# Kernel tuning notes

Hardware: AMD Instinct MI355X
Metric: run time of the kernel (lower is better)

Reference implementation:

```python
import jax, jax.numpy as jnp
import numpy as np

EMB_DIM = 1024
N_HEADS = 16
HEAD_DIM = EMB_DIM // N_HEADS
WINDOW = 128
B, T = 4, 2048


def setup_inputs() -> dict:
    key = jax.random.key(0)
    k1, k2, k3 = jax.random.split(key, 3)
    x = jax.random.normal(k1, (B, T, EMB_DIM), dtype=jnp.float32)
    # nn.Linear weights: stored as [out, in], applied as x @ W^T
    s1 = 1.0 / np.sqrt(EMB_DIM)
    w_qkv = jax.random.uniform(k2, (3 * EMB_DIM, EMB_DIM), jnp.float32, -s1, s1)
    w_out = jax.random.uniform(k3, (EMB_DIM, EMB_DIM), jnp.float32, -s1, s1)
    return {"x": x, "w_qkv": w_qkv, "w_out": w_out}


def reference(x, w_qkv, w_out):
    Bs, Ts, C = x.shape
    scale = HEAD_DIM ** -0.5
    qkv = x @ w_qkv.T                                   # [B,T,3C]
    qkv = qkv.reshape(Bs, Ts, 3, N_HEADS, HEAD_DIM)
    qkv = jnp.transpose(qkv, (2, 0, 3, 1, 4))           # [3,B,H,T,D]
    q, k, v = qkv[0], qkv[1], qkv[2]
    scores = jnp.einsum('bhtd,bhsd->bhts', q, k) * scale  # [B,H,T,T]
    i = jnp.arange(Ts)[:, None]
    j = jnp.arange(Ts)[None, :]
    # causal AND within sliding window: i - WINDOW <= j <= i
    allowed = (j <= i) & (j >= i - WINDOW)               # [T,T] bool
    scores = jnp.where(allowed[None, None], scores, -jnp.inf)
    attn = jax.nn.softmax(scores, axis=-1)
    out = jnp.einsum('bhts,bhsd->bhtd', attn, v)         # [B,H,T,D]
    out = jnp.transpose(out, (0, 2, 1, 3)).reshape(Bs, Ts, C)
    return out @ w_out.T
```

## Files before the change

kernel.cpp:

```cpp
#include <hip/hip_runtime.h>
#include <hip/hip_bf16.h>
#include <stdint.h>

typedef __attribute__((ext_vector_type(8))) short bf16x8;
typedef __attribute__((ext_vector_type(4))) float f32x4;
typedef __attribute__((ext_vector_type(4))) unsigned short u16x4;

#define B_ 4
#define T_ 2048
#define C_ 1024
#define H_ 16
#define D_ 64

__device__ __forceinline__ unsigned short f2bf(float f) {
  union { float f; uint32_t u; } v; v.f = f;
  uint32_t u = v.u;
  uint32_t r = (u + 0x7FFFu + ((u >> 16) & 1u)) >> 16;
  return (unsigned short)r;
}

__global__ void __launch_bounds__(256) cast_all(const float* __restrict__ x,
                                                const float* __restrict__ wqkv,
                                                const float* __restrict__ wout,
                                                unsigned short* __restrict__ xb,
                                                unsigned short* __restrict__ wqkvb,
                                                unsigned short* __restrict__ woutb) {
  int bid = blockIdx.x;
  const float* src; unsigned short* dst; int i;
  if (bid < 8192)       { src = x;    dst = xb;    i = bid * 256 + threadIdx.x; }
  else if (bid < 11264) { src = wqkv; dst = wqkvb; i = (bid - 8192) * 256 + threadIdx.x; }
  else                  { src = wout; dst = woutb; i = (bid - 11264) * 256 + threadIdx.x; }
  float4 f = ((const float4*)src)[i];
  u16x4 o;
  o[0] = f2bf(f.x); o[1] = f2bf(f.y); o[2] = f2bf(f.z); o[3] = f2bf(f.w);
  ((u16x4*)dst)[i] = o;
}

__global__ void __launch_bounds__(256, 2) gemm_qkv(const unsigned short* __restrict__ A,
                                                   const unsigned short* __restrict__ Bm,
                                                   unsigned short* __restrict__ qb,
                                                   unsigned short* __restrict__ kb,
                                                   unsigned short* __restrict__ vb) {
  __shared__ short lds[24576];
  const int tid = threadIdx.x;
  const int bm = blockIdx.y * 256;
  const int bn = blockIdx.x * 128;

  const int wave = tid >> 6;
  const int l = tid & 63;
  const int wm = wave >> 1, wn = wave & 1;
  const int lm = l & 15, lq = l >> 4;
  const int lr = l >> 2;
  const int lc = (l & 3) << 3;

  f32x4 acc[8][4];
#pragma unroll
  for (int i = 0; i < 8; i++)
#pragma unroll
    for (int j = 0; j < 4; j++) acc[i][j] = (f32x4){0.f, 0.f, 0.f, 0.f};

  const unsigned short* gs[6];
  int ldo[6];
#pragma unroll
  for (int i = 0; i < 6; i++) {
    int c = wave * 6 + i;
    if (c < 16) {
      gs[i] = A + (size_t)(bm + 16 * c + lr) * 1024 + lc;
      ldo[i] = c * 512;
    } else {
      gs[i] = Bm + (size_t)(bn + 16 * (c - 16) + lr) * 1024 + lc;
      ldo[i] = 8192 + (c - 16) * 512;
    }
  }

#define STAGE(curb, kk)                                                          \
  do {                                                                           \
    _Pragma("unroll")                                                            \
    for (int i = 0; i < 6; i++) {                                                \
      __builtin_amdgcn_global_load_lds(                                          \
          (__attribute__((address_space(1))) void*)(uintptr_t)(const void*)(gs[i] + (kk)), \
          (__attribute__((address_space(3))) void*)(lds + ldo[i] + (curb) * 12288),        \
          16, 0, 0);                                                             \
    }                                                                            \
  } while (0)

  STAGE(0, 0);
  int cur = 0;
  __syncthreads();

  for (int k0 = 0; k0 < 1024; k0 += 32) {
    if (k0 + 32 < 1024) STAGE(cur ^ 1, k0 + 32);
    const short* As_ = lds + cur * 12288;
    const short* Bs_ = lds + cur * 12288 + 8192;
    bf16x8 Bf[4];
#pragma unroll
    for (int j = 0; j < 4; j++)
      Bf[j] = *(const bf16x8*)&Bs_[(wn * 64 + 16 * j + lm) * 32 + 8 * lq];
#pragma unroll
    for (int h = 0; h < 2; h++) {
      bf16x8 Af[4];
#pragma unroll
      for (int i = 0; i < 4; i++)
        Af[i] = *(const bf16x8*)&As_[(wm * 128 + 64 * h + 16 * i + lm) * 32 + 8 * lq];
#pragma unroll
      for (int i = 0; i < 4; i++)
#pragma unroll
        for (int j = 0; j < 4; j++)
          acc[4 * h + i][j] =
              __builtin_amdgcn_mfma_f32_16x16x32_bf16(Af[i], Bf[j], acc[4 * h + i][j], 0, 0, 0);
    }
    __syncthreads();
    cur ^= 1;
  }
#undef STAGE

  if (bn >= 2048) {
#pragma unroll
    for (int h = 0; h < 2; h++)
#pragma unroll
      for (int i = 0; i < 4; i++)
#pragma unroll
        for (int j = 0; j < 4; j++) {
          int m0 = bm + wm * 128 + 64 * h + 16 * i + 4 * lq;
          int n = (bn - 2048) + wn * 64 + 16 * j + lm;
          int hh = n >> 6, d = n & 63;
          int b = m0 >> 11, t = m0 & 2047;
          u16x4 o;
#pragma unroll
          for (int r = 0; r < 4; r++) o[r] = f2bf(acc[4 * h + i][j][r]);
          *(u16x4*)&vb[(((size_t)(b * 16 + hh)) * 64 + d) * 2048 + t] = o;
        }
  } else {
#pragma unroll
    for (int p = 0; p < 2; ++p) {
      if (p) __syncthreads();
      if (wm == p) {
#pragma unroll
        for (int h = 0; h < 2; h++)
#pragma unroll
          for (int i = 0; i < 4; i++)
#pragma unroll
            for (int j = 0; j < 4; j++)
#pragma unroll
              for (int r = 0; r < 4; r++)
                lds[(64 * h + 16 * i + 4 * lq + r) * 132 + wn * 64 + 16 * j + lm] =
                    (short)f2bf(acc[4 * h + i][j][r]);
      }
      __syncthreads();
#pragma unroll
      for (int k = 0; k < 8; k++) {
        int c = tid + 256 * k;
        int row = c >> 4;
        int col = (c & 15) << 3;
        bf16x8 v = *(const bf16x8*)&lds[row * 132 + col];
        int m = bm + 128 * p + row, n = bn + col;
        int which = n >> 10, rem = n & 1023;
        int hh = rem >> 6, d = rem & 63;
        int b = m >> 11, t = m & 2047;
        unsigned short* dst = (which == 0) ? qb : kb;
        *(bf16x8*)&dst[(((size_t)(b * 16 + hh)) * 2048 + t) * 64 + d] = v;
      }
    }
  }
}

__global__ void __launch_bounds__(256) gemm_out(const unsigned short* __restrict__ A,
                                                const unsigned short* __restrict__ Bm,
                                                float* __restrict__ fo) {
  __shared__ short lds[16384];
  const int tid = threadIdx.x;
  const int bm = blockIdx.y * 128;
  const int bn = blockIdx.x * 128;
  const int wave = tid >> 6;
  const int l = tid & 63;
  const int wm = wave >> 1, wn = wave & 1;
  const int lm = l & 15, lq = l >> 4;
  const int lr = l >> 2;
  const int lc = (l & 3) << 3;

  f32x4 acc[4][4];
#pragma unroll
  for (int i = 0; i < 4; i++)
#pragma unroll
    for (int j = 0; j < 4; j++) acc[i][j] = (f32x4){0.f, 0.f, 0.f, 0.f};

  const unsigned short* gsrc[4];
  int ldoff[4];
#pragma unroll
  for (int i = 0; i < 4; i++) {
    int c = wave * 4 + i;
    if (c < 8) {
      gsrc[i] = A + (size_t)(bm + 16 * c + lr) * 1024 + lc;
      ldoff[i] = (16 * c) * 32;
    } else {
      gsrc[i] = Bm + (size_t)(bn + 16 * (c - 8) + lr) * 1024 + lc;
      ldoff[i] = 8192 + (16 * (c - 8)) * 32;
    }
  }

#define STAGE(curb, kk)                                                          \
  do {                                                                           \
    _Pragma("unroll")                                                            \
    for (int i = 0; i < 4; i++) {                                                \
      __builtin_amdgcn_global_load_lds(                                          \
          (__attribute__((address_space(1))) void*)(uintptr_t)(const void*)(gsrc[i] + (kk)), \
          (__attribute__((address_space(3))) void*)(lds + ldoff[i] + (curb) * 4096),         \
          16, 0, 0);                                                             \
    }                                                                            \
  } while (0)

  STAGE(0, 0);
  int cur = 0;
  __syncthreads();

  for (int k0 = 0; k0 < 1024; k0 += 32) {
    if (k0 + 32 < 1024) STAGE(cur ^ 1, k0 + 32);
    bf16x8 af[4], bfr[4];
#pragma unroll
    for (int i = 0; i < 4; i++)
      af[i] = *(const bf16x8*)&lds[cur * 4096 + (wm * 64 + 16 * i + lm) * 32 + 8 * lq];
#pragma unroll
    for (int j = 0; j < 4; j++)
      bfr[j] = *(const bf16x8*)&lds[8192 + cur * 4096 + (wn * 64 + 16 * j + lm) * 32 + 8 * lq];
#pragma unroll
    for (int i = 0; i < 4; i++)
#pragma unroll
      for (int j = 0; j < 4; j++)
        acc[i][j] = __builtin_amdgcn_mfma_f32_16x16x32_bf16(af[i], bfr[j], acc[i][j], 0, 0, 0);
    __syncthreads();
    cur ^= 1;
  }
#undef STAGE

#pragma unroll
  for (int i = 0; i < 4; i++)
#pragma unroll
    for (int j = 0; j < 4; j++)
#pragma unroll
      for (int r = 0; r < 4; r++) {
        int m = bm + wm * 64 + 16 * i + 4 * lq + r;
        int n = bn + wn * 64 + 16 * j + lm;
        fo[(size_t)m * 1024 + n] = acc[i][j][r];
      }
}

__global__ void __launch_bounds__(256) attn_swa(const unsigned short* __restrict__ Qb,
                                               const unsigned short* __restrict__ Kb,
                                               const unsigned short* __restrict__ Vt,
                                               unsigned short* __restrict__ Ob) {
  __shared__ short P[4][16 * 40];
  const int wv = threadIdx.x >> 6;
  const int l = threadIdx.x & 63;
  const int wid = blockIdx.x * 4 + wv;
  const int bh = wid >> 7;
  const int t0 = (wid & 127) << 4;
  const int lm = l & 15, lq = l >> 4;
  const size_t base = (size_t)bh * (T_ * D_);

  bf16x8 aq0 = *(const bf16x8*)(Qb + base + (size_t)(t0 + lm) * 64 + 8 * lq);
  bf16x8 aq1 = *(const bf16x8*)(Qb + base + (size_t)(t0 + lm) * 64 + 32 + 8 * lq);

  float mst[4], lst[4];
  f32x4 Oa[4];
#pragma unroll
  for (int r = 0; r < 4; r++) { mst[r] = -1e30f; lst[r] = 0.f; }
#pragma unroll
  for (int jt = 0; jt < 4; jt++) Oa[jt] = (f32x4){0.f, 0.f, 0.f, 0.f};

  const float cs = 0.125f * 1.44269504f;
  int jstart = t0 - 128; if (jstart < 0) jstart = 0;

  for (int j0 = jstart; j0 < t0 + 16; j0 += 32) {
    f32x4 S[2];
#pragma unroll
    for (int hh = 0; hh < 2; hh++) {
      int kr = j0 + 16 * hh + lm; if (kr > T_ - 1) kr = T_ - 1;
      bf16x8 bk0 = *(const bf16x8*)(Kb + base + (size_t)kr * 64 + 8 * lq);
      bf16x8 bk1 = *(const bf16x8*)(Kb + base + (size_t)kr * 64 + 32 + 8 * lq);
      f32x4 s = (f32x4){0.f, 0.f, 0.f, 0.f};
      s = __builtin_amdgcn_mfma_f32_16x16x32_bf16(aq0, bk0, s, 0, 0, 0);
      s = __builtin_amdgcn_mfma_f32_16x16x32_bf16(aq1, bk1, s, 0, 0, 0);
      S[hh] = s;
    }
    float p0s[4], p1s[4], al[4];
#pragma unroll
    for (int r = 0; r < 4; r++) {
      int t = t0 + 4 * lq + r;
      int ja = j0 + lm, jb = j0 + 16 + lm;
      float s0 = ((ja <= t) && (ja + 128 >= t)) ? S[0][r] * cs : -1e30f;
      float s1 = ((jb <= t) && (jb + 128 >= t)) ? S[1][r] * cs : -1e30f;
      float m2 = fmaxf(s0, s1);
#pragma unroll
      for (int off = 1; off < 16; off <<= 1) m2 = fmaxf(m2, __shfl_xor(m2, off));
      float mn = fmaxf(mst[r], m2);
      float a = __builtin_amdgcn_exp2f(mst[r] - mn);
      float p0 = __builtin_amdgcn_exp2f(s0 - mn);
      float p1 = __builtin_amdgcn_exp2f(s1 - mn);
      float ps = p0 + p1;
#pragma unroll
      for (int off = 1; off < 16; off <<= 1) ps += __shfl_xor(ps, off);
      lst[r] = lst[r] * a + ps;
      mst[r] = mn;
      al[r] = a; p0s[r] = p0; p1s[r] = p1;
    }
#pragma unroll
    for (int jt = 0; jt < 4; jt++)
#pragma unroll
      for (int r = 0; r < 4; r++) Oa[jt][r] *= al[r];
#pragma unroll
    for (int r = 0; r < 4; r++) {
      P[wv][(4 * lq + r) * 40 + lm] = (short)f2bf(p0s[r]);
      P[wv][(4 * lq + r) * 40 + 16 + lm] = (short)f2bf(p1s[r]);
    }
    bf16x8 pa = *(const bf16x8*)&P[wv][lm * 40 + 8 * lq];
#pragma unroll
    for (int jt = 0; jt < 4; jt++) {
      bf16x8 vf = *(const bf16x8*)(Vt + base + (size_t)(16 * jt + lm) * 2048 + j0 + 8 * lq);
      Oa[jt] = __builtin_amdgcn_mfma_f32_16x16x32_bf16(pa, vf, Oa[jt], 0, 0, 0);
    }
  }
  const int b = bh >> 4, h = bh & 15;
#pragma unroll
  for (int r = 0; r < 4; r++) {
    float inv = 1.0f / lst[r];
    int t = t0 + 4 * lq + r;
#pragma unroll
    for (int jt = 0; jt < 4; jt++) {
      int c = h * 64 + 16 * jt + lm;
      Ob[((size_t)(b * T_ + t)) * 1024 + c] = f2bf(Oa[jt][r] * inv);
    }
  }
}

extern "C" void kernel_launch(void* const* d_in, const int* in_sizes, int n_in,
                              void* d_out, int out_size, void* d_ws, size_t ws_size,
                              hipStream_t stream) {
  const float* x = (const float*)d_in[0];
  const float* w_qkv = (const float*)d_in[1];
  const float* w_out = (const float*)d_in[2];
  float* out = (float*)d_out;

  unsigned short* xb = (unsigned short*)d_ws;
  unsigned short* wqkvb = xb + (size_t)8192 * 1024;
  unsigned short* woutb = wqkvb + (size_t)3072 * 1024;
  unsigned short* qb = woutb + (size_t)1024 * 1024;
  unsigned short* kb = qb + (size_t)64 * 2048 * 64;
  unsigned short* vb = kb + (size_t)64 * 2048 * 64;

  cast_all<<<12288, 256, 0, stream>>>(x, w_qkv, w_out, xb, wqkvb, woutb);

  gemm_qkv<<<dim3(24, 32), 256, 0, stream>>>(xb, wqkvb, qb, kb, vb);

  attn_swa<<<2048, 256, 0, stream>>>(qb, kb, vb, xb);

  gemm_out<<<dim3(8, 64), 256, 0, stream>>>(xb, woutb, out);
}
```

Before: 229.9 us.

## Process four query tiles per wave in sliding-window attention to reuse K/V loads

Each attention wave now handles 64 query rows as four 16-row tiles instead of one, so every loaded K and V fragment feeds up to four MFMA tiles, with per-tile activity masks skipping fully masked tiles. This cuts redundant global K/V reads but raises register pressure and shrinks the grid to 512 blocks, which may lower occupancy. The QKV GEMM launch is also split into two half-height launches via a row-offset argument, which adds a launch without an obvious speed benefit.

```diff
diff --git a/kernel.cpp b/kernel.cpp
--- a/kernel.cpp
+++ b/kernel.cpp
@@ -40,10 +40,11 @@
                                                    const unsigned short* __restrict__ Bm,
                                                    unsigned short* __restrict__ qb,
                                                    unsigned short* __restrict__ kb,
-                                                   unsigned short* __restrict__ vb) {
+                                                   unsigned short* __restrict__ vb,
+                                                   int bm0) {
   __shared__ short lds[24576];
   const int tid = threadIdx.x;
-  const int bm = blockIdx.y * 256;
+  const int bm = bm0 + blockIdx.y * 256;
   const int bn = blockIdx.x * 128;
 
   const int wave = tid >> 6;
@@ -248,88 +249,119 @@
                                                const unsigned short* __restrict__ Kb,
                                                const unsigned short* __restrict__ Vt,
                                                unsigned short* __restrict__ Ob) {
-  __shared__ short P[4][16 * 40];
+  __shared__ short P[4][64 * 40];
   const int wv = threadIdx.x >> 6;
   const int l = threadIdx.x & 63;
   const int wid = blockIdx.x * 4 + wv;
-  const int bh = wid >> 7;
-  const int t0 = (wid & 127) << 4;
+  const int bh = wid >> 5;
+  const int t0 = (wid & 31) << 6;
   const int lm = l & 15, lq = l >> 4;
   const size_t base = (size_t)bh * (T_ * D_);
 
-  bf16x8 aq0 = *(const bf16x8*)(Qb + base + (size_t)(t0 + lm) * 64 + 8 * lq);
-  bf16x8 aq1 = *(const bf16x8*)(Qb + base + (size_t)(t0 + lm) * 64 + 32 + 8 * lq);
-
-  float mst[4], lst[4];
-  f32x4 Oa[4];
-#pragma unroll
-  for (int r = 0; r < 4; r++) { mst[r] = -1e30f; lst[r] = 0.f; }
-#pragma unroll
-  for (int jt = 0; jt < 4; jt++) Oa[jt] = (f32x4){0.f, 0.f, 0.f, 0.f};
+  bf16x8 aq[4][2];
+#pragma unroll
+  for (int qt = 0; qt < 4; qt++) {
+    aq[qt][0] = *(const bf16x8*)(Qb + base + (size_t)(t0 + 16 * qt + lm) * 64 + 8 * lq);
+    aq[qt][1] = *(const bf16x8*)(Qb + base + (size_t)(t0 + 16 * qt + lm) * 64 + 32 + 8 * lq);
+  }
+
+  float mst[4][4], lst[4][4];
+  f32x4 Oa[4][4];
+#pragma unroll
+  for (int qt = 0; qt < 4; qt++)
+#pragma unroll
+    for (int r = 0; r < 4; r++) { mst[qt][r] = -1e30f; lst[qt][r] = 0.f; }
+#pragma unroll
+  for (int qt = 0; qt < 4; qt++)
+#pragma unroll
+    for (int jt = 0; jt < 4; jt++) Oa[qt][jt] = (f32x4){0.f, 0.f, 0.f, 0.f};
 
   const float cs = 0.125f * 1.44269504f;
   int jstart = t0 - 128; if (jstart < 0) jstart = 0;
 
-  for (int j0 = jstart; j0 < t0 + 16; j0 += 32) {
-    f32x4 S[2];
+  for (int j0 = jstart; j0 < t0 + 64; j0 += 32) {
+    bool act[4];
+#pragma unroll
+    for (int qt = 0; qt < 4; qt++) {
+      int t0q = t0 + 16 * qt;
+      act[qt] = (j0 <= t0q + 15) && (j0 + 159 >= t0q);
+    }
+    f32x4 S[4][2];
 #pragma unroll
     for (int hh = 0; hh < 2; hh++) {
-      int kr = j0 + 16 * hh + lm; if (kr > T_ - 1) kr = T_ - 1;
-      bf16x8 bk0 = *(const bf16x8*)(Kb + base + (size_t)kr * 64 + 8 * lq);
-      bf16x8 bk1 = *(const bf16x8*)(Kb + base + (size_t)kr * 64 + 32 + 8 * lq);
-      f32x4 s = (f32x4){0.f, 0.f, 0.f, 0.f};
-      s = __builtin_amdgcn_mfma_f32_16x16x32_bf16(aq0, bk0, s, 0, 0, 0);
-      s = __builtin_amdgcn_mfma_f32_16x16x32_bf16(aq1, bk1, s, 0, 0, 0);
-      S[hh] = s;
-    }
-    float p0s[4], p1s[4], al[4];
+      int kr = j0 + 16 * hh + lm;
+      bf16x8 bkA = *(const bf16x8*)(Kb + base + (size_t)kr * 64 + 8 * lq);
+      bf16x8 bkB = *(const bf16x8*)(Kb + base + (size_t)kr * 64 + 32 + 8 * lq);
+#pragma unroll
+      for (int qt = 0; qt < 4; qt++)
+        if (act[qt]) {
+          f32x4 s = (f32x4){0.f, 0.f, 0.f, 0.f};
+          s = __builtin_amdgcn_mfma_f32_16x16x32_bf16(aq[qt][0], bkA, s, 0, 0, 0);
+          s = __builtin_amdgcn_mfma_f32_16x16x32_bf16(aq[qt][1], bkB, s, 0, 0, 0);
+          S[qt][hh] = s;
+        }
+    }
+#pragma unroll
+    for (int qt = 0; qt < 4; qt++)
+      if (act[qt]) {
+        int t0q = t0 + 16 * qt;
+        float p0s[4], p1s[4], al[4];
+#pragma unroll
+        for (int r = 0; r < 4; r++) {
+          int t = t0q + 4 * lq + r;
+          int ja = j0 + lm, jb = j0 + 16 + lm;
+          float s0 = ((ja <= t) && (ja + 128 >= t)) ? S[qt][0][r] * cs : -1e30f;
+          float s1 = ((jb <= t) && (jb + 128 >= t)) ? S[qt][1][r] * cs : -1e30f;
+          float m2 = fmaxf(s0, s1);
+#pragma unroll
+          for (int off = 1; off < 16; off <<= 1) m2 = fmaxf(m2, __shfl_xor(m2, off));
+          float mn = fmaxf(mst[qt][r], m2);
+          float a = __builtin_amdgcn_exp2f(mst[qt][r] - mn);
+          float p0 = (s0 > -1e29f) ? __builtin_amdgcn_exp2f(s0 - mn) : 0.f;
+          float p1 = (s1 > -1e29f) ? __builtin_amdgcn_exp2f(s1 - mn) : 0.f;
+          float ps = p0 + p1;
+#pragma unroll
+          for (int off = 1; off < 16; off <<= 1) ps += __shfl_xor(ps, off);
+          lst[qt][r] = lst[qt][r] * a + ps;
+          mst[qt][r] = mn;
+          al[r] = a; p0s[r] = p0; p1s[r] = p1;
+        }
+#pragma unroll
+        for (int jt = 0; jt < 4; jt++)
+#pragma unroll
+          for (int r = 0; r < 4; r++) Oa[qt][jt][r] *= al[r];
+#pragma unroll
+        for (int r = 0; r < 4; r++) {
+          P[wv][(qt * 16 + 4 * lq + r) * 40 + lm] = (short)f2bf(p0s[r]);
+          P[wv][(qt * 16 + 4 * lq + r) * 40 + 16 + lm] = (short)f2bf(p1s[r]);
+        }
+      }
+    bf16x8 vf[4];
+#pragma unroll
+    for (int jt = 0; jt < 4; jt++)
+      vf[jt] = *(const bf16x8*)(Vt + base + (size_t)(16 * jt + lm) * 2048 + j0 + 8 * lq);
+#pragma unroll
+    for (int qt = 0; qt < 4; qt++)
+      if (act[qt]) {
+        bf16x8 pa = *(const bf16x8*)&P[wv][(qt * 16 + lm) * 40 + 8 * lq];
+#pragma unroll
+        for (int jt = 0; jt < 4; jt++)
+          Oa[qt][jt] = __builtin_amdgcn_mfma_f32_16x16x32_bf16(pa, vf[jt], Oa[qt][jt], 0, 0, 0);
+      }
+  }
+  const int b = bh >> 4, h = bh & 15;
+#pragma unroll
+  for (int qt = 0; qt < 4; qt++)
 #pragma unroll
     for (int r = 0; r < 4; r++) {
-      int t = t0 + 4 * lq + r;
-      int ja = j0 + lm, jb = j0 + 16 + lm;
-      float s0 = ((ja <= t) && (ja + 128 >= t)) ? S[0][r] * cs : -1e30f;
-      float s1 = ((jb <= t) && (jb + 128 >= t)) ? S[1][r] * cs : -1e30f;
-      float m2 = fmaxf(s0, s1);
-#pragma unroll
-      for (int off = 1; off < 16; off <<= 1) m2 = fmaxf(m2, __shfl_xor(m2, off));
-      float mn = fmaxf(mst[r], m2);
-      float a = __builtin_amdgcn_exp2f(mst[r] - mn);
-      float p0 = __builtin_amdgcn_exp2f(s0 - mn);
-      float p1 = __builtin_amdgcn_exp2f(s1 - mn);
-      float ps = p0 + p1;
-#pragma unroll
-      for (int off = 1; off < 16; off <<= 1) ps += __shfl_xor(ps, off);
-      lst[r] = lst[r] * a + ps;
-      mst[r] = mn;
-      al[r] = a; p0s[r] = p0; p1s[r] = p1;
-    }
-#pragma unroll
-    for (int jt = 0; jt < 4; jt++)
-#pragma unroll
-      for (int r = 0; r < 4; r++) Oa[jt][r] *= al[r];
-#pragma unroll
-    for (int r = 0; r < 4; r++) {
-      P[wv][(4 * lq + r) * 40 + lm] = (short)f2bf(p0s[r]);
-      P[wv][(4 * lq + r) * 40 + 16 + lm] = (short)f2bf(p1s[r]);
-    }
-    bf16x8 pa = *(const bf16x8*)&P[wv][lm * 40 + 8 * lq];
-#pragma unroll
-    for (int jt = 0; jt < 4; jt++) {
-      bf16x8 vf = *(const bf16x8*)(Vt + base + (size_t)(16 * jt + lm) * 2048 + j0 + 8 * lq);
-      Oa[jt] = __builtin_amdgcn_mfma_f32_16x16x32_bf16(pa, vf, Oa[jt], 0, 0, 0);
-    }
-  }
-  const int b = bh >> 4, h = bh & 15;
-#pragma unroll
-  for (int r = 0; r < 4; r++) {
-    float inv = 1.0f / lst[r];
-    int t = t0 + 4 * lq + r;
-#pragma unroll
-    for (int jt = 0; jt < 4; jt++) {
-      int c = h * 64 + 16 * jt + lm;
-      Ob[((size_t)(b * T_ + t)) * 1024 + c] = f2bf(Oa[jt][r] * inv);
-    }
-  }
+      float inv = 1.0f / lst[qt][r];
+      int t = t0 + 16 * qt + 4 * lq + r;
+#pragma unroll
+      for (int jt = 0; jt < 4; jt++) {
+        int c = h * 64 + 16 * jt + lm;
+        Ob[((size_t)(b * T_ + t)) * 1024 + c] = f2bf(Oa[qt][jt][r] * inv);
+      }
+    }
 }
 
 extern "C" void kernel_launch(void* const* d_in, const int* in_sizes, int n_in,
@@ -349,9 +381,10 @@
 
   cast_all<<<12288, 256, 0, stream>>>(x, w_qkv, w_out, xb, wqkvb, woutb);
 
-  gemm_qkv<<<dim3(24, 32), 256, 0, stream>>>(xb, wqkvb, qb, kb, vb);
-
-  attn_swa<<<2048, 256, 0, stream>>>(qb, kb, vb, xb);
+  gemm_qkv<<<dim3(24, 16), 256, 0, stream>>>(xb, wqkvb, qb, kb, vb, 0);
+  gemm_qkv<<<dim3(24, 16), 256, 0, stream>>>(xb, wqkvb, qb, kb, vb, 4096);
+
+  attn_swa<<<512, 256, 0, stream>>>(qb, kb, vb, xb);
 
   gemm_out<<<dim3(8, 64), 256, 0, stream>>>(xb, woutb, out);
 }
```

Result: slower. 249.9 us (+8.7%).

## Process two query tiles per wave and compute transposed scores in attention

Applied to the files above, without the earlier changes.

Each wave now handles 32 query rows instead of 16, loading the K and V fragments once per 32-key step and reusing them across both query tiles, with half as many blocks launched. Scores are computed as K·Q^T so each lane holds one query column, which turns the row max/sum reductions into two cross-quadrant shuffles instead of four, with the rescale factors broadcast by shuffle. Masked entries are zeroed explicitly, and P is written with packed 4-wide LDS stores into a padded 48-wide buffer. The trade is more registers per wave (hence the launch-bounds occupancy hint) and fewer waves overall.

```diff
diff --git a/kernel.cpp b/kernel.cpp
--- a/kernel.cpp
+++ b/kernel.cpp
@@ -244,90 +244,119 @@
       }
 }
 
-__global__ void __launch_bounds__(256) attn_swa(const unsigned short* __restrict__ Qb,
-                                               const unsigned short* __restrict__ Kb,
-                                               const unsigned short* __restrict__ Vt,
-                                               unsigned short* __restrict__ Ob) {
-  __shared__ short P[4][16 * 40];
+__global__ void __launch_bounds__(256, 4) attn_swa(const unsigned short* __restrict__ Qb,
+                                                   const unsigned short* __restrict__ Kb,
+                                                   const unsigned short* __restrict__ Vt,
+                                                   unsigned short* __restrict__ Ob) {
+  __shared__ short P[4][16 * 48];
   const int wv = threadIdx.x >> 6;
   const int l = threadIdx.x & 63;
   const int wid = blockIdx.x * 4 + wv;
-  const int bh = wid >> 7;
-  const int t0 = (wid & 127) << 4;
+  const int bh = wid >> 6;
+  const int t0 = (wid & 63) << 5;
   const int lm = l & 15, lq = l >> 4;
   const size_t base = (size_t)bh * (T_ * D_);
 
-  bf16x8 aq0 = *(const bf16x8*)(Qb + base + (size_t)(t0 + lm) * 64 + 8 * lq);
-  bf16x8 aq1 = *(const bf16x8*)(Qb + base + (size_t)(t0 + lm) * 64 + 32 + 8 * lq);
-
-  float mst[4], lst[4];
-  f32x4 Oa[4];
-#pragma unroll
-  for (int r = 0; r < 4; r++) { mst[r] = -1e30f; lst[r] = 0.f; }
-#pragma unroll
-  for (int jt = 0; jt < 4; jt++) Oa[jt] = (f32x4){0.f, 0.f, 0.f, 0.f};
+  bf16x8 qf[2][2];
+#pragma unroll
+  for (int qt = 0; qt < 2; qt++) {
+    qf[qt][0] = *(const bf16x8*)(Qb + base + (size_t)(t0 + 16 * qt + lm) * 64 + 8 * lq);
+    qf[qt][1] = *(const bf16x8*)(Qb + base + (size_t)(t0 + 16 * qt + lm) * 64 + 32 + 8 * lq);
+  }
+
+  float mst[2] = {-1e30f, -1e30f}, lst[2] = {0.f, 0.f};
+  f32x4 Oa[2][4];
+#pragma unroll
+  for (int qt = 0; qt < 2; qt++)
+#pragma unroll
+    for (int jt = 0; jt < 4; jt++) Oa[qt][jt] = (f32x4){0.f, 0.f, 0.f, 0.f};
 
   const float cs = 0.125f * 1.44269504f;
   int jstart = t0 - 128; if (jstart < 0) jstart = 0;
 
-  for (int j0 = jstart; j0 < t0 + 16; j0 += 32) {
-    f32x4 S[2];
+  for (int j0 = jstart; j0 < t0 + 32; j0 += 32) {
+    bf16x8 ka[2][2];
 #pragma unroll
     for (int hh = 0; hh < 2; hh++) {
-      int kr = j0 + 16 * hh + lm; if (kr > T_ - 1) kr = T_ - 1;
-      bf16x8 bk0 = *(const bf16x8*)(Kb + base + (size_t)kr * 64 + 8 * lq);
-      bf16x8 bk1 = *(const bf16x8*)(Kb + base + (size_t)kr * 64 + 32 + 8 * lq);
-      f32x4 s = (f32x4){0.f, 0.f, 0.f, 0.f};
-      s = __builtin_amdgcn_mfma_f32_16x16x32_bf16(aq0, bk0, s, 0, 0, 0);
-      s = __builtin_amdgcn_mfma_f32_16x16x32_bf16(aq1, bk1, s, 0, 0, 0);
-      S[hh] = s;
-    }
-    float p0s[4], p1s[4], al[4];
+      int kr = j0 + 16 * hh + lm;
+      ka[hh][0] = *(const bf16x8*)(Kb + base + (size_t)kr * 64 + 8 * lq);
+      ka[hh][1] = *(const bf16x8*)(Kb + base + (size_t)kr * 64 + 32 + 8 * lq);
+    }
+    bf16x8 vf[4];
+#pragma unroll
+    for (int jt = 0; jt < 4; jt++)
+      vf[jt] = *(const bf16x8*)(Vt + base + (size_t)(16 * jt + lm) * 2048 + j0 + 8 * lq);
+
+#pragma unroll
+    for (int qt = 0; qt < 2; qt++) {
+      const int t0q = t0 + 16 * qt;
+      const int t = t0q + lm;
+      f32x4 s0 = (f32x4){0.f, 0.f, 0.f, 0.f}, s1 = (f32x4){0.f, 0.f, 0.f, 0.f};
+      s0 = __builtin_amdgcn_mfma_f32_16x16x32_bf16(ka[0][0], qf[qt][0], s0, 0, 0, 0);
+      s0 = __builtin_amdgcn_mfma_f32_16x16x32_bf16(ka[0][1], qf[qt][1], s0, 0, 0, 0);
+      s1 = __builtin_amdgcn_mfma_f32_16x16x32_bf16(ka[1][0], qf[qt][0], s1, 0, 0, 0);
+      s1 = __builtin_amdgcn_mfma_f32_16x16x32_bf16(ka[1][1], qf[qt][1], s1, 0, 0, 0);
+      float sv[8];
+      float m2 = -1e30f;
+#pragma unroll
+      for (int hh = 0; hh < 2; hh++)
+#pragma unroll
+        for (int r = 0; r < 4; r++) {
+          int k = j0 + 16 * hh + 4 * lq + r;
+          float x = (hh ? s1[r] : s0[r]) * cs;
+          bool okm = (k <= t) && (k + 128 >= t);
+          sv[hh * 4 + r] = okm ? x : -1e30f;
+          m2 = fmaxf(m2, sv[hh * 4 + r]);
+        }
+      m2 = fmaxf(m2, __shfl_xor(m2, 16));
+      m2 = fmaxf(m2, __shfl_xor(m2, 32));
+      float mn = fmaxf(mst[qt], m2);
+      float a = __builtin_amdgcn_exp2f(mst[qt] - mn);
+      float ps = 0.f;
+#pragma unroll
+      for (int i = 0; i < 8; i++) {
+        sv[i] = (sv[i] > -1e29f) ? __builtin_amdgcn_exp2f(sv[i] - mn) : 0.f;
+        ps += sv[i];
+      }
+      ps += __shfl_xor(ps, 16);
+      ps += __shfl_xor(ps, 32);
+      lst[qt] = lst[qt] * a + ps;
+      mst[qt] = mn;
+#pragma unroll
+      for (int hh = 0; hh < 2; hh++) {
+        u16x4 pk;
+#pragma unroll
+        for (int r = 0; r < 4; r++) pk[r] = f2bf(sv[hh * 4 + r]);
+        *(u16x4*)&P[wv][lm * 48 + 16 * hh + 4 * lq] = pk;
+      }
+      float al[4];
+#pragma unroll
+      for (int r = 0; r < 4; r++) al[r] = __shfl(a, 4 * lq + r);
+#pragma unroll
+      for (int jt = 0; jt < 4; jt++)
+#pragma unroll
+        for (int r = 0; r < 4; r++) Oa[qt][jt][r] *= al[r];
+      bf16x8 pa = *(const bf16x8*)&P[wv][lm * 48 + 8 * lq];
+#pragma unroll
+      for (int jt = 0; jt < 4; jt++)
+        Oa[qt][jt] = __builtin_amdgcn_mfma_f32_16x16x32_bf16(pa, vf[jt], Oa[qt][jt], 0, 0, 0);
+    }
+  }
+  const int b = bh >> 4, h = bh & 15;
+#pragma unroll
+  for (int qt = 0; qt < 2; qt++) {
+    float inv = 1.0f / lst[qt];
+    float invl[4];
+#pragma unroll
+    for (int r = 0; r < 4; r++) invl[r] = __shfl(inv, 4 * lq + r);
 #pragma unroll
     for (int r = 0; r < 4; r++) {
-      int t = t0 + 4 * lq + r;
-      int ja = j0 + lm, jb = j0 + 16 + lm;
-      float s0 = ((ja <= t) && (ja + 128 >= t)) ? S[0][r] * cs : -1e30f;
-      float s1 = ((jb <= t) && (jb + 128 >= t)) ? S[1][r] * cs : -1e30f;
-      float m2 = fmaxf(s0, s1);
-#pragma unroll
-      for (int off = 1; off < 16; off <<= 1) m2 = fmaxf(m2, __shfl_xor(m2, off));
-      float mn = fmaxf(mst[r], m2);
-      float a = __builtin_amdgcn_exp2f(mst[r] - mn);
-      float p0 = __builtin_amdgcn_exp2f(s0 - mn);
-      float p1 = __builtin_amdgcn_exp2f(s1 - mn);
-      float ps = p0 + p1;
-#pragma unroll
-      for (int off = 1; off < 16; off <<= 1) ps += __shfl_xor(ps, off);
-      lst[r] = lst[r] * a + ps;
-      mst[r] = mn;
-      al[r] = a; p0s[r] = p0; p1s[r] = p1;
-    }
-#pragma unroll
-    for (int jt = 0; jt < 4; jt++)
-#pragma unroll
-      for (int r = 0; r < 4; r++) Oa[jt][r] *= al[r];
-#pragma unroll
-    for (int r = 0; r < 4; r++) {
-      P[wv][(4 * lq + r) * 40 + lm] = (short)f2bf(p0s[r]);
-      P[wv][(4 * lq + r) * 40 + 16 + lm] = (short)f2bf(p1s[r]);
-    }
-    bf16x8 pa = *(const bf16x8*)&P[wv][lm * 40 + 8 * lq];
-#pragma unroll
-    for (int jt = 0; jt < 4; jt++) {
-      bf16x8 vf = *(const bf16x8*)(Vt + base + (size_t)(16 * jt + lm) * 2048 + j0 + 8 * lq);
-      Oa[jt] = __builtin_amdgcn_mfma_f32_16x16x32_bf16(pa, vf, Oa[jt], 0, 0, 0);
-    }
-  }
-  const int b = bh >> 4, h = bh & 15;
-#pragma unroll
-  for (int r = 0; r < 4; r++) {
-    float inv = 1.0f / lst[r];
-    int t = t0 + 4 * lq + r;
-#pragma unroll
-    for (int jt = 0; jt < 4; jt++) {
-      int c = h * 64 + 16 * jt + lm;
-      Ob[((size_t)(b * T_ + t)) * 1024 + c] = f2bf(Oa[jt][r] * inv);
+      int t = t0 + 16 * qt + 4 * lq + r;
+#pragma unroll
+      for (int jt = 0; jt < 4; jt++) {
+        int c = h * 64 + 16 * jt + lm;
+        Ob[((size_t)(b * T_ + t)) * 1024 + c] = f2bf(Oa[qt][jt][r] * invl[r]);
+      }
     }
   }
 }
@@ -351,7 +380,7 @@
 
   gemm_qkv<<<dim3(24, 32), 256, 0, stream>>>(xb, wqkvb, qb, kb, vb);
 
-  attn_swa<<<2048, 256, 0, stream>>>(qb, kb, vb, xb);
+  attn_swa<<<1024, 256, 0, stream>>>(qb, kb, vb, xb);
 
   gemm_out<<<dim3(8, 64), 256, 0, stream>>>(xb, woutb, out);
 }
```

Result: faster. 216.4 us (-5.9%).
